# Kernel optimization log

Hardware: AMD Instinct MI355X
Metric: run time of the kernel (lower is better)

The kernel has to match this reference:

```python
import jax, jax.numpy as jnp
import numpy as np

CHAN = 128
IN_CHAN = 3
NB_OUT = 10
K = 2  # maxPoolKer


def affine_grid(theta, H, W):
    # theta: [C,2,3] -> grid [C,H,W,2], torch F.affine_grid align_corners=False
    xs = (2.0 * jnp.arange(W, dtype=jnp.float32) + 1.0) / W - 1.0
    ys = (2.0 * jnp.arange(H, dtype=jnp.float32) + 1.0) / H - 1.0
    gx, gy = jnp.meshgrid(xs, ys)  # [H,W]
    base = jnp.stack([gx, gy, jnp.ones_like(gx)], axis=-1)  # [H,W,3]
    return jnp.einsum('crk,hwk->chwr', theta, base)  # [...,0]=x, [...,1]=y


def grid_sample(img, grid):
    # img [M,H,W], grid [M,H,W,2]; bilinear, zeros padding, align_corners=False
    M, H, W = img.shape
    ix = ((grid[..., 0] + 1.0) * W - 1.0) * 0.5
    iy = ((grid[..., 1] + 1.0) * H - 1.0) * 0.5
    x0 = jnp.floor(ix)
    y0 = jnp.floor(iy)
    wx = ix - x0
    wy = iy - y0

    def tap(xi, yi):
        valid = (xi >= 0) & (xi <= W - 1) & (yi >= 0) & (yi <= H - 1)
        xc = jnp.clip(xi, 0, W - 1).astype(jnp.int32)
        yc = jnp.clip(yi, 0, H - 1).astype(jnp.int32)
        v = jax.vmap(lambda im, y, x: im[y, x])(img, yc, xc)
        return jnp.where(valid, v, 0.0)

    v00 = tap(x0, y0)
    v01 = tap(x0 + 1.0, y0)
    v10 = tap(x0, y0 + 1.0)
    v11 = tap(x0 + 1.0, y0 + 1.0)
    return (1.0 - wy) * ((1.0 - wx) * v00 + wx * v01) + wy * ((1.0 - wx) * v10 + wx * v11)


def geom_layer(x, geo, lin, box):
    # x [B,Ci,H,W]; lin [C,Ci]; geo,box [C,2,3]
    B, Ci, H, W = x.shape
    C = lin.shape[0]
    y = jnp.einsum('ci,bihw->bchw', lin, x)  # channel linear combine
    grid = affine_grid(geo, H, W)            # [C,H,W,2], shared across batch
    samp = jax.vmap(lambda yb: grid_sample(yb, grid))(y)  # [B,C,H,W]
    bgrid = affine_grid(box, H, W)
    boxm = grid_sample(jnp.ones((C, H, W), samp.dtype), bgrid)  # BoxPool mask
    return samp * boxm[None]


def maxpool_g(x, k):
    # MaxPool2d_G: depthwise box-filter conv -> argmax -> gather window from padded x
    B, C, H, W = x.shape
    ch, cw = H // k, W // k
    ker = jnp.ones((1, 1, ch, cw), x.dtype) / (ch + cw)
    xr = x.reshape(B * C, 1, H, W)
    conv = jax.lax.conv_general_dilated(
        xr, ker, (1, 1), [(ch // 2, ch // 2), (cw // 2, cw // 2)])
    conv = conv[:, :, :H, :W].reshape(B, C, H * W)
    argm = jnp.argmax(conv, axis=-1)
    r = argm // H  # original code uses origImgSize[0]; assumes square H==W
    c = argm % W
    padH, padW = H + H // k, W + W // k
    top = padH // 2 - H // 2
    left = padW // 2 - W // 2
    padded = jnp.zeros((B, C, padH, padW), x.dtype).at[:, :, top:top + H, left:left + W].set(x)
    r2 = r + H // (2 * k)
    c2 = c + W // (2 * k)
    ri = r2[..., None] + (jnp.arange(ch) - ch // 2)  # [B,C,ch]
    ci = c2[..., None] + (jnp.arange(cw) - cw // 2)  # [B,C,cw]
    gat = jax.vmap(jax.vmap(lambda p, rr, cc: p[rr[:, None], cc[None, :]]))(padded, ri, ci)
    return gat  # [B,C,ch,cw]


def setup_inputs() -> dict:
    key = jax.random.key(0)
    ks = jax.random.split(key, 12)
    eye = jnp.eye(3, dtype=jnp.float32)[:2]  # [2,3]
    x = jax.random.normal(ks[0], (8, IN_CHAN, 64, 64), dtype=jnp.float32)
    geo0 = eye[None] + 0.1 * jax.random.normal(ks[1], (CHAN, 2, 3), dtype=jnp.float32)
    lin0 = jax.random.uniform(ks[2], (CHAN, IN_CHAN), dtype=jnp.float32)
    box0 = eye[None] + 0.1 * jax.random.normal(ks[3], (CHAN, 2, 3), dtype=jnp.float32)
    geos = eye[None, None] + 0.1 * jax.random.normal(ks[4], (3, CHAN, 2, 3), dtype=jnp.float32)
    lins = jax.random.uniform(ks[5], (3, CHAN, CHAN), dtype=jnp.float32)
    boxes = eye[None, None] + 0.1 * jax.random.normal(ks[6], (3, CHAN, 2, 3), dtype=jnp.float32)
    bound = 1.0 / np.sqrt(CHAN)
    dense_w = jax.random.uniform(ks[7], (NB_OUT, CHAN), dtype=jnp.float32, minval=-bound, maxval=bound)
    dense_b = jax.random.uniform(ks[8], (NB_OUT,), dtype=jnp.float32, minval=-bound, maxval=bound)
    return {"x": x, "geo0": geo0, "lin0": lin0, "box0": box0,
            "geos": geos, "lins": lins, "boxes": boxes,
            "dense_w": dense_w, "dense_b": dense_b}


def reference(x, geo0, lin0, box0, geos, lins, boxes, dense_w, dense_b):
    h = geom_layer(x, geo0, lin0, box0)            # inLay: [8,128,64,64]
    h = geom_layer(h, geos[0], lins[0], boxes[0])  # layer 0
    h = maxpool_g(h, K)                            # layer 1 (maxPoolPos=1): [8,128,32,32]
    h = geom_layer(h, geos[1], lins[1], boxes[1])  # layer 2
    h = geom_layer(h, geos[2], lins[2], boxes[2])  # layer 3
    feat = h
    pooled = feat.mean(axis=-1).mean(axis=-1)      # [B,C]
    out = pooled @ dense_w.T + dense_b             # [B,nbOut]
    return out, feat
```

## Files before the change

kernel.cpp:

```cpp
#include <hip/hip_runtime.h>

#define BB 8
#define CC 128

__global__ __launch_bounds__(256) void inlay_sample_kernel(
    const float* __restrict__ x, const float* __restrict__ lin,
    const float* __restrict__ geo, const float* __restrict__ box,
    float* __restrict__ out) {
  const int H = 64, W = 64, HW = 4096;
  __shared__ __align__(16) float cp[64 * 68];
  int bc = blockIdx.x;
  int c = bc & (CC - 1);
  int b = bc >> 7;
  int tid = threadIdx.x;
  const float* xb = x + (size_t)b * 3 * HW;

  float w0 = lin[c * 3 + 0], w1 = lin[c * 3 + 1], w2 = lin[c * 3 + 2];

#pragma unroll
  for (int k = 0; k < 4; ++k) {
    int i4 = tid + k * 256;
    int base = i4 * 4;
    float4 f0 = *reinterpret_cast<const float4*>(&xb[base]);
    float4 f1 = *reinterpret_cast<const float4*>(&xb[HW + base]);
    float4 f2 = *reinterpret_cast<const float4*>(&xb[2 * HW + base]);
    float4 cv;
    cv.x = w0 * f0.x + w1 * f1.x + w2 * f2.x;
    cv.y = w0 * f0.y + w1 * f1.y + w2 * f2.y;
    cv.z = w0 * f0.z + w1 * f1.z + w2 * f2.z;
    cv.w = w0 * f0.w + w1 * f1.w + w2 * f2.w;
    int h = i4 >> 4, w = (i4 & 15) * 4;
    *reinterpret_cast<float4*>(&cp[h * 68 + w]) = cv;
  }
  __syncthreads();

  const float* g = geo + c * 6;
  const float* bx = box + c * 6;
  float g0 = g[0], g1 = g[1], g2 = g[2], g3 = g[3], g4 = g[4], g5 = g[5];
  float b0 = bx[0], b1 = bx[1], b2 = bx[2], b3 = bx[3], b4 = bx[4], b5 = bx[5];
  float* o = out + ((size_t)b * CC + c) * HW;

#pragma unroll
  for (int k = 0; k < 16; ++k) {
    int px = tid + k * 256;
    int h = px >> 6, w = px & 63;
    float xs = (2.0f * w + 1.0f) / W - 1.0f;
    float ys = (2.0f * h + 1.0f) / H - 1.0f;
    float gx = g0 * xs + g1 * ys + g2;
    float gy = g3 * xs + g4 * ys + g5;
    float ix = ((gx + 1.0f) * W - 1.0f) * 0.5f;
    float iy = ((gy + 1.0f) * H - 1.0f) * 0.5f;
    float x0 = floorf(ix), y0 = floorf(iy);
    float wx = ix - x0, wy = iy - y0;
    float v[2][2];
#pragma unroll
    for (int dy = 0; dy < 2; ++dy)
#pragma unroll
      for (int dx = 0; dx < 2; ++dx) {
        float xf = x0 + dx, yf = y0 + dy;
        bool valid = (xf >= 0.0f) && (xf <= 63.0f) && (yf >= 0.0f) && (yf <= 63.0f);
        int xi = (int)fminf(fmaxf(xf, 0.0f), 63.0f);
        int yi = (int)fminf(fmaxf(yf, 0.0f), 63.0f);
        v[dy][dx] = valid ? cp[yi * 68 + xi] : 0.0f;
      }
    float samp = (1.0f - wy) * ((1.0f - wx) * v[0][0] + wx * v[0][1]) +
                 wy * ((1.0f - wx) * v[1][0] + wx * v[1][1]);

    float bgx = b0 * xs + b1 * ys + b2;
    float bgy = b3 * xs + b4 * ys + b5;
    float bix = ((bgx + 1.0f) * W - 1.0f) * 0.5f;
    float biy = ((bgy + 1.0f) * H - 1.0f) * 0.5f;
    float bx0 = floorf(bix), by0 = floorf(biy);
    float bwx = bix - bx0, bwy = biy - by0;
    float m[2][2];
#pragma unroll
    for (int dy = 0; dy < 2; ++dy)
#pragma unroll
      for (int dx = 0; dx < 2; ++dx) {
        float xf = bx0 + dx, yf = by0 + dy;
        m[dy][dx] = ((xf >= 0.0f) && (xf <= 63.0f) && (yf >= 0.0f) && (yf <= 63.0f)) ? 1.0f : 0.0f;
      }
    float mask = (1.0f - bwy) * ((1.0f - bwx) * m[0][0] + bwx * m[0][1]) +
                 bwy * ((1.0f - bwx) * m[1][0] + bwx * m[1][1]);
    o[px] = samp * mask;
  }
}

__global__ __launch_bounds__(256) void gemm64_kernel(
    const float* __restrict__ lin, const float* __restrict__ x,
    float* __restrict__ y, int HW) {
  const int Ci = 128;
  __shared__ __align__(16) float As[16][68];
  __shared__ __align__(16) float Bs[16][64];
  int b = blockIdx.z;
  const float* xb = x + (size_t)b * Ci * HW;
  float* yb = y + (size_t)b * CC * HW;
  int tid = threadIdx.x;
  int tx = tid & 15, ty = tid >> 4;
  int row0 = blockIdx.y * 64;
  int col0 = blockIdx.x * 64;
  int m = tid >> 2, kq = (tid & 3) * 4;
  int kk = tid >> 4, n4 = (tid & 15) * 4;
  float acc[4][4] = {};
  float4 ra = *reinterpret_cast<const float4*>(&lin[(row0 + m) * Ci + kq]);
  float4 rb = *reinterpret_cast<const float4*>(&xb[(size_t)kk * HW + col0 + n4]);
  for (int k0 = 0; k0 < 128; k0 += 16) {
    __syncthreads();
    As[kq + 0][m] = ra.x; As[kq + 1][m] = ra.y; As[kq + 2][m] = ra.z; As[kq + 3][m] = ra.w;
    *reinterpret_cast<float4*>(&Bs[kk][n4]) = rb;
    __syncthreads();
    if (k0 + 16 < 128) {
      ra = *reinterpret_cast<const float4*>(&lin[(row0 + m) * Ci + k0 + 16 + kq]);
      rb = *reinterpret_cast<const float4*>(&xb[(size_t)(k0 + 16 + kk) * HW + col0 + n4]);
    }
#pragma unroll
    for (int kki = 0; kki < 16; ++kki) {
      float4 a4 = *reinterpret_cast<const float4*>(&As[kki][ty * 4]);
      float4 b4 = *reinterpret_cast<const float4*>(&Bs[kki][tx * 4]);
      float a[4] = {a4.x, a4.y, a4.z, a4.w};
      float bv[4] = {b4.x, b4.y, b4.z, b4.w};
#pragma unroll
      for (int i = 0; i < 4; i++)
#pragma unroll
        for (int j = 0; j < 4; j++) acc[i][j] += a[i] * bv[j];
    }
  }
#pragma unroll
  for (int i = 0; i < 4; i++) {
    float* yr = yb + (size_t)(row0 + ty * 4 + i) * HW + col0 + tx * 4;
    *reinterpret_cast<float4*>(yr) = make_float4(acc[i][0], acc[i][1], acc[i][2], acc[i][3]);
  }
}

__global__ __launch_bounds__(1024, 4) void sampmax_kernel(
    const float* __restrict__ y, const float* __restrict__ geo,
    const float* __restrict__ box, float* __restrict__ out) {
  __shared__ __align__(16) float sp[64 * 68];
  __shared__ __align__(16) float arena[64 * 100];
  __shared__ float wv[16];
  __shared__ int wi[16];
  __shared__ int am_s;
  float* pl = arena;
  float* cb = arena;

  int bc = blockIdx.x;
  int c = bc & (CC - 1);
  int b = bc >> 7;
  int tid = threadIdx.x;

  const float* plane = y + (size_t)bc * 4096;
  *reinterpret_cast<float4*>(&pl[tid * 4]) = *reinterpret_cast<const float4*>(&plane[tid * 4]);
  __syncthreads();

  {
    const float* g = geo + c * 6;
    const float* bx = box + c * 6;
    float g0 = g[0], g1 = g[1], g2 = g[2], g3 = g[3], g4 = g[4], g5 = g[5];
    float b0 = bx[0], b1 = bx[1], b2 = bx[2], b3 = bx[3], b4 = bx[4], b5 = bx[5];
#pragma unroll
    for (int k = 0; k < 4; ++k) {
      int px = tid + k * 1024;
      int h = px >> 6, w = px & 63;
      float xs = (2.0f * w + 1.0f) / 64.0f - 1.0f;
      float ys = (2.0f * h + 1.0f) / 64.0f - 1.0f;
      float gx = g0 * xs + g1 * ys + g2;
      float gy = g3 * xs + g4 * ys + g5;
      float ix = ((gx + 1.0f) * 64.0f - 1.0f) * 0.5f;
      float iy = ((gy + 1.0f) * 64.0f - 1.0f) * 0.5f;
      float x0 = floorf(ix), y0 = floorf(iy);
      float wx = ix - x0, wy = iy - y0;
      float v[2][2];
#pragma unroll
      for (int dy = 0; dy < 2; ++dy)
#pragma unroll
        for (int dx = 0; dx < 2; ++dx) {
          float xf = x0 + dx, yf = y0 + dy;
          bool valid = (xf >= 0.0f) && (xf <= 63.0f) && (yf >= 0.0f) && (yf <= 63.0f);
          int xi = (int)fminf(fmaxf(xf, 0.0f), 63.0f);
          int yi = (int)fminf(fmaxf(yf, 0.0f), 63.0f);
          v[dy][dx] = valid ? pl[yi * 64 + xi] : 0.0f;
        }
      float samp = (1.0f - wy) * ((1.0f - wx) * v[0][0] + wx * v[0][1]) +
                   wy * ((1.0f - wx) * v[1][0] + wx * v[1][1]);
      float bgx = b0 * xs + b1 * ys + b2;
      float bgy = b3 * xs + b4 * ys + b5;
      float bix = ((bgx + 1.0f) * 64.0f - 1.0f) * 0.5f;
      float biy = ((bgy + 1.0f) * 64.0f - 1.0f) * 0.5f;
      float bx0 = floorf(bix), by0 = floorf(biy);
      float bwx = bix - bx0, bwy = biy - by0;
      float m[2][2];
#pragma unroll
      for (int dy = 0; dy < 2; ++dy)
#pragma unroll
        for (int dx = 0; dx < 2; ++dx) {
          float xf = bx0 + dx, yf = by0 + dy;
          m[dy][dx] = ((xf >= 0.0f) && (xf <= 63.0f) && (yf >= 0.0f) && (yf <= 63.0f)) ? 1.0f : 0.0f;
        }
      float mask = (1.0f - bwy) * ((1.0f - bwx) * m[0][0] + bwx * m[0][1]) +
                   bwy * ((1.0f - bwx) * m[1][0] + bwx * m[1][1]);
      sp[h * 68 + w] = samp * mask;
    }
  }
  __syncthreads();

  if (tid < 256) {
    int strip = tid >> 4, w4 = (tid & 15) * 4;
    int h0 = strip * 4;
    float4 a0 = make_float4(0.f, 0.f, 0.f, 0.f), a1 = a0, a2 = a0, a3 = a0;
#pragma unroll
    for (int j = 0; j < 35; ++j) {
      int r = h0 + j - 16;
      bool valid = (r >= 0) && (r < 64);
      int rc = valid ? r : 0;
      float4 f = *reinterpret_cast<const float4*>(&sp[rc * 68 + w4]);
      f.x = valid ? f.x : 0.0f; f.y = valid ? f.y : 0.0f;
      f.z = valid ? f.z : 0.0f; f.w = valid ? f.w : 0.0f;
      if (j <= 31) { a0.x += f.x; a0.y += f.y; a0.z += f.z; a0.w += f.w; }
      if (j >= 1 && j <= 32) { a1.x += f.x; a1.y += f.y; a1.z += f.z; a1.w += f.w; }
      if (j >= 2 && j <= 33) { a2.x += f.x; a2.y += f.y; a2.z += f.z; a2.w += f.w; }
      if (j >= 3) { a3.x += f.x; a3.y += f.y; a3.z += f.z; a3.w += f.w; }
    }
    *reinterpret_cast<float4*>(&cb[(h0 + 0) * 100 + 16 + w4]) = a0;
    *reinterpret_cast<float4*>(&cb[(h0 + 1) * 100 + 16 + w4]) = a1;
    *reinterpret_cast<float4*>(&cb[(h0 + 2) * 100 + 16 + w4]) = a2;
    *reinterpret_cast<float4*>(&cb[(h0 + 3) * 100 + 16 + w4]) = a3;
  } else if (tid < 768) {
    int l = tid - 256;
    int row = l >> 3, gq = l & 7;
    int base = row * 100 + ((gq < 4) ? gq * 4 : 80 + (gq - 4) * 4);
    *reinterpret_cast<float4*>(&cb[base]) = make_float4(0.f, 0.f, 0.f, 0.f);
  }
  __syncthreads();

  float best = -3.402823466e+38f;
  int bidx = 0x7fffffff;
  {
    int h = tid >> 4, w4 = (tid & 15) * 4;
    float s0 = 0.f, s1 = 0.f, s2 = 0.f, s3 = 0.f;
#pragma unroll
    for (int q = 0; q < 9; ++q) {
      float4 f = *reinterpret_cast<const float4*>(&cb[h * 100 + w4 + 4 * q]);
      float fe[4] = {f.x, f.y, f.z, f.w};
#pragma unroll
      for (int e = 0; e < 4; ++e) {
        int u = 4 * q + e;
        if (u <= 31) s0 += fe[e];
        if (u >= 1 && u <= 32) s1 += fe[e];
        if (u >= 2 && u <= 33) s2 += fe[e];
        if (u >= 3 && u <= 34) s3 += fe[e];
      }
    }
    float sv[4] = {s0, s1, s2, s3};
#pragma unroll
    for (int d = 0; d < 4; ++d) {
      int i = (h << 6) + w4 + d;
      if (sv[d] > best) { best = sv[d]; bidx = i; }
    }
  }
#pragma unroll
  for (int off = 32; off > 0; off >>= 1) {
    float v2 = __shfl_down(best, off);
    int i2 = __shfl_down(bidx, off);
    if (v2 > best || (v2 == best && i2 < bidx)) { best = v2; bidx = i2; }
  }
  if ((tid & 63) == 0) { wv[tid >> 6] = best; wi[tid >> 6] = bidx; }
  __syncthreads();
  if (tid == 0) {
    float bv = wv[0]; int bi = wi[0];
#pragma unroll
    for (int k = 1; k < 16; ++k)
      if (wv[k] > bv || (wv[k] == bv && wi[k] < bi)) { bv = wv[k]; bi = wi[k]; }
    am_s = bi;
  }
  __syncthreads();

  int am = am_s;
  int r = am >> 6, cx = am & 63;
  float* o = out + (size_t)bc * 1024;
  {
    int oi = tid >> 5, oj = tid & 31;
    int rr = r + oi - 16, cj = cx + oj - 16;
    bool v = (rr >= 0) && (rr < 64) && (cj >= 0) && (cj < 64);
    int rrc = v ? rr : 0, cjc = v ? cj : 0;
    o[tid] = v ? sp[rrc * 68 + cjc] : 0.0f;
  }
}

template <bool POOL>
__global__ __launch_bounds__(256) void fused32_kernel(
    const float* __restrict__ lin, const float* __restrict__ x,
    const float* __restrict__ geo, const float* __restrict__ box,
    float* __restrict__ out, float* __restrict__ pooled) {
  const int H = 32, W = 32, HW = 1024;
  __shared__ __align__(16) float pls[2][1024];
  __shared__ float wred[8];
  int b = blockIdx.x & 7;
  int c0 = (blockIdx.x >> 3) * 2;
  int tid = threadIdx.x;
  const float* xb = x + (size_t)b * 128 * HW;
  const float* l0 = lin + (c0 + 0) * 128;
  const float* l1 = lin + (c0 + 1) * 128;
  int px4 = tid * 4;

  float4 acc0 = make_float4(0.f, 0.f, 0.f, 0.f);
  float4 acc1 = acc0;
#pragma unroll 8
  for (int k = 0; k < 128; ++k) {
    float4 xv = *reinterpret_cast<const float4*>(&xb[(size_t)k * HW + px4]);
    float s0 = l0[k], s1 = l1[k];
    acc0.x += s0 * xv.x; acc0.y += s0 * xv.y; acc0.z += s0 * xv.z; acc0.w += s0 * xv.w;
    acc1.x += s1 * xv.x; acc1.y += s1 * xv.y; acc1.z += s1 * xv.z; acc1.w += s1 * xv.w;
  }
  *reinterpret_cast<float4*>(&pls[0][px4]) = acc0;
  *reinterpret_cast<float4*>(&pls[1][px4]) = acc1;
  __syncthreads();

  float psum[2] = {0.f, 0.f};
#pragma unroll
  for (int c = 0; c < 2; ++c) {
    const float* g = geo + (c0 + c) * 6;
    const float* bxp = box + (c0 + c) * 6;
    float g0 = g[0], g1 = g[1], g2 = g[2], g3 = g[3], g4 = g[4], g5 = g[5];
    float b0 = bxp[0], b1 = bxp[1], b2 = bxp[2], b3 = bxp[3], b4 = bxp[4], b5 = bxp[5];
    float* o = out + ((size_t)b * CC + c0 + c) * HW;
    const float* pl = pls[c];
#pragma unroll
    for (int k = 0; k < 4; ++k) {
      int px = tid + k * 256;
      int h = px >> 5, w = px & 31;
      float xs = (2.0f * w + 1.0f) / W - 1.0f;
      float ys = (2.0f * h + 1.0f) / H - 1.0f;
      float gx = g0 * xs + g1 * ys + g2;
      float gy = g3 * xs + g4 * ys + g5;
      float ix = ((gx + 1.0f) * W - 1.0f) * 0.5f;
      float iy = ((gy + 1.0f) * H - 1.0f) * 0.5f;
      float x0 = floorf(ix), y0 = floorf(iy);
      float wx = ix - x0, wy = iy - y0;
      float v[2][2];
#pragma unroll
      for (int dy = 0; dy < 2; ++dy)
#pragma unroll
        for (int dx = 0; dx < 2; ++dx) {
          float xf = x0 + dx, yf = y0 + dy;
          bool valid = (xf >= 0.0f) && (xf <= 31.0f) && (yf >= 0.0f) && (yf <= 31.0f);
          int xi = (int)fminf(fmaxf(xf, 0.0f), 31.0f);
          int yi = (int)fminf(fmaxf(yf, 0.0f), 31.0f);
          v[dy][dx] = valid ? pl[yi * 32 + xi] : 0.0f;
        }
      float samp = (1.0f - wy) * ((1.0f - wx) * v[0][0] + wx * v[0][1]) +
                   wy * ((1.0f - wx) * v[1][0] + wx * v[1][1]);
      float bgx = b0 * xs + b1 * ys + b2;
      float bgy = b3 * xs + b4 * ys + b5;
      float bix = ((bgx + 1.0f) * W - 1.0f) * 0.5f;
      float biy = ((bgy + 1.0f) * H - 1.0f) * 0.5f;
      float bx0 = floorf(bix), by0 = floorf(biy);
      float bwx = bix - bx0, bwy = biy - by0;
      float m[2][2];
#pragma unroll
      for (int dy = 0; dy < 2; ++dy)
#pragma unroll
        for (int dx = 0; dx < 2; ++dx) {
          float xf = bx0 + dx, yf = by0 + dy;
          m[dy][dx] = ((xf >= 0.0f) && (xf <= 31.0f) && (yf >= 0.0f) && (yf <= 31.0f)) ? 1.0f : 0.0f;
        }
      float mask = (1.0f - bwy) * ((1.0f - bwx) * m[0][0] + bwx * m[0][1]) +
                   bwy * ((1.0f - bwx) * m[1][0] + bwx * m[1][1]);
      float res = samp * mask;
      o[px] = res;
      if (POOL) psum[c] += res;
    }
  }
  if (POOL) {
    int lane = tid & 63, wid = tid >> 6;
#pragma unroll
    for (int c = 0; c < 2; ++c) {
      float r = psum[c];
#pragma unroll
      for (int off = 32; off > 0; off >>= 1) r += __shfl_down(r, off);
      if (lane == 0) wred[c * 4 + wid] = r;
    }
    __syncthreads();
    if (tid < 2) {
      float t = wred[tid * 4] + wred[tid * 4 + 1] + wred[tid * 4 + 2] + wred[tid * 4 + 3];
      pooled[b * CC + c0 + tid] = t * (1.0f / 1024.0f);
    }
  }
}

__global__ __launch_bounds__(128) void dense_kernel(
    const float* __restrict__ pooled, const float* __restrict__ w,
    const float* __restrict__ bias, float* __restrict__ out) {
  int t = threadIdx.x;
  if (t < 80) {
    int b = t / 10, o = t % 10;
    float s = bias[o];
    const float* pb = pooled + b * 128;
    const float* wo = w + o * 128;
    for (int c = 0; c < 128; ++c) s += pb[c] * wo[c];
    out[b * 10 + o] = s;
  }
}

extern "C" void kernel_launch(void* const* d_in, const int* in_sizes, int n_in,
                              void* d_out, int out_size, void* d_ws, size_t ws_size,
                              hipStream_t stream) {
  const float* x     = (const float*)d_in[0];
  const float* geo0  = (const float*)d_in[1];
  const float* lin0  = (const float*)d_in[2];
  const float* box0  = (const float*)d_in[3];
  const float* geos  = (const float*)d_in[4];
  const float* lins  = (const float*)d_in[5];
  const float* boxes = (const float*)d_in[6];
  const float* dw    = (const float*)d_in[7];
  const float* db    = (const float*)d_in[8];

  float* out  = (float*)d_out;
  float* feat = out + 80;
  float* ws   = (float*)d_ws;
  float* ws0  = ws;
  float* ws1  = ws + 4194304;
  float* pooled = ws + 8388608;

  inlay_sample_kernel<<<dim3(BB * CC), 256, 0, stream>>>(x, lin0, geo0, box0, ws1);
  gemm64_kernel<<<dim3(64, 2, BB), 256, 0, stream>>>(lins, ws1, ws0, 4096);
  sampmax_kernel<<<dim3(BB * CC), 1024, 0, stream>>>(ws0, geos, boxes, ws1);
  fused32_kernel<false><<<dim3(512), 256, 0, stream>>>(lins + 16384, ws1, geos + 768, boxes + 768, ws0, nullptr);
  fused32_kernel<true><<<dim3(512), 256, 0, stream>>>(lins + 32768, ws0, geos + 1536, boxes + 1536, feat, pooled);
  dense_kernel<<<1, 128, 0, stream>>>(pooled, dw, db, out);
}
```

Before: 163.2 us.

## Fuse dense head via atomics, sliding-window box filter, remap block indices, 4-channel fused32

Removes the separate dense kernel. The inlay kernel now seeds the output with the bias, and the last fused32 kernel adds per-channel pooled contributions through atomicAdd. The box-filter in sampmax now uses sliding-window subtraction instead of four masked accumulators. Block indices are remapped so that batch varies fastest across inlay, gemm and sampmax, and fused32 now handles four channels per 512-thread block using float2 loads. The atomics make the summation order nondeterministic, and the head output depends on the inlay kernel running first to write the bias.

Measured after the change: 167.9 us. 2.9% more time.

```diff
diff --git a/kernel.cpp b/kernel.cpp
--- a/kernel.cpp
+++ b/kernel.cpp
@@ -6,13 +6,15 @@
 __global__ __launch_bounds__(256) void inlay_sample_kernel(
     const float* __restrict__ x, const float* __restrict__ lin,
     const float* __restrict__ geo, const float* __restrict__ box,
-    float* __restrict__ out) {
+    const float* __restrict__ db, float* __restrict__ out,
+    float* __restrict__ head) {
   const int H = 64, W = 64, HW = 4096;
   __shared__ __align__(16) float cp[64 * 68];
   int bc = blockIdx.x;
-  int c = bc & (CC - 1);
-  int b = bc >> 7;
+  int b = bc & 7;
+  int c = bc >> 3;
   int tid = threadIdx.x;
+  if (bc == 0 && tid < 80) head[tid] = db[tid % 10];
   const float* xb = x + (size_t)b * 3 * HW;
 
   float w0 = lin[c * 3 + 0], w1 = lin[c * 3 + 1], w2 = lin[c * 3 + 2];
@@ -92,13 +94,15 @@
   const int Ci = 128;
   __shared__ __align__(16) float As[16][68];
   __shared__ __align__(16) float Bs[16][64];
-  int b = blockIdx.z;
+  int bx = blockIdx.x;
+  int b = bx & 7;
+  int t = bx >> 3;
+  int row0 = (t & 1) * 64;
+  int col0 = (t >> 1) * 64;
   const float* xb = x + (size_t)b * Ci * HW;
   float* yb = y + (size_t)b * CC * HW;
   int tid = threadIdx.x;
   int tx = tid & 15, ty = tid >> 4;
-  int row0 = blockIdx.y * 64;
-  int col0 = blockIdx.x * 64;
   int m = tid >> 2, kq = (tid & 3) * 4;
   int kk = tid >> 4, n4 = (tid & 15) * 4;
   float acc[4][4] = {};
@@ -144,11 +148,11 @@
   float* cb = arena;
 
   int bc = blockIdx.x;
-  int c = bc & (CC - 1);
-  int b = bc >> 7;
+  int b = bc & 7;
+  int c = bc >> 3;
   int tid = threadIdx.x;
 
-  const float* plane = y + (size_t)bc * 4096;
+  const float* plane = y + ((size_t)b * CC + c) * 4096;
   *reinterpret_cast<float4*>(&pl[tid * 4]) = *reinterpret_cast<const float4*>(&plane[tid * 4]);
   __syncthreads();
 
@@ -206,24 +210,34 @@
   if (tid < 256) {
     int strip = tid >> 4, w4 = (tid & 15) * 4;
     int h0 = strip * 4;
-    float4 a0 = make_float4(0.f, 0.f, 0.f, 0.f), a1 = a0, a2 = a0, a3 = a0;
-#pragma unroll
-    for (int j = 0; j < 35; ++j) {
+    float4 a = make_float4(0.f, 0.f, 0.f, 0.f);
+    float4 keep0 = a, keep1 = a, keep2 = a;
+#pragma unroll
+    for (int j = 0; j < 32; ++j) {
       int r = h0 + j - 16;
       bool valid = (r >= 0) && (r < 64);
       int rc = valid ? r : 0;
       float4 f = *reinterpret_cast<const float4*>(&sp[rc * 68 + w4]);
       f.x = valid ? f.x : 0.0f; f.y = valid ? f.y : 0.0f;
       f.z = valid ? f.z : 0.0f; f.w = valid ? f.w : 0.0f;
-      if (j <= 31) { a0.x += f.x; a0.y += f.y; a0.z += f.z; a0.w += f.w; }
-      if (j >= 1 && j <= 32) { a1.x += f.x; a1.y += f.y; a1.z += f.z; a1.w += f.w; }
-      if (j >= 2 && j <= 33) { a2.x += f.x; a2.y += f.y; a2.z += f.z; a2.w += f.w; }
-      if (j >= 3) { a3.x += f.x; a3.y += f.y; a3.z += f.z; a3.w += f.w; }
-    }
-    *reinterpret_cast<float4*>(&cb[(h0 + 0) * 100 + 16 + w4]) = a0;
-    *reinterpret_cast<float4*>(&cb[(h0 + 1) * 100 + 16 + w4]) = a1;
-    *reinterpret_cast<float4*>(&cb[(h0 + 2) * 100 + 16 + w4]) = a2;
-    *reinterpret_cast<float4*>(&cb[(h0 + 3) * 100 + 16 + w4]) = a3;
+      if (j == 0) keep0 = f;
+      if (j == 1) keep1 = f;
+      if (j == 2) keep2 = f;
+      a.x += f.x; a.y += f.y; a.z += f.z; a.w += f.w;
+    }
+    *reinterpret_cast<float4*>(&cb[(h0 + 0) * 100 + 16 + w4]) = a;
+#pragma unroll
+    for (int j = 32; j < 35; ++j) {
+      int r = h0 + j - 16;
+      bool valid = (r < 64);
+      int rc = valid ? r : 0;
+      float4 f = *reinterpret_cast<const float4*>(&sp[rc * 68 + w4]);
+      f.x = valid ? f.x : 0.0f; f.y = valid ? f.y : 0.0f;
+      f.z = valid ? f.z : 0.0f; f.w = valid ? f.w : 0.0f;
+      float4 kp = (j == 32) ? keep0 : ((j == 33) ? keep1 : keep2);
+      a.x += f.x - kp.x; a.y += f.y - kp.y; a.z += f.z - kp.z; a.w += f.w - kp.w;
+      *reinterpret_cast<float4*>(&cb[(h0 + j - 31) * 100 + 16 + w4]) = a;
+    }
   } else if (tid < 768) {
     int l = tid - 256;
     int row = l >> 3, gq = l & 7;
@@ -236,20 +250,17 @@
   int bidx = 0x7fffffff;
   {
     int h = tid >> 4, w4 = (tid & 15) * 4;
-    float s0 = 0.f, s1 = 0.f, s2 = 0.f, s3 = 0.f;
-#pragma unroll
-    for (int q = 0; q < 9; ++q) {
+    float s0 = 0.f, k0 = 0.f, k1 = 0.f, k2 = 0.f;
+#pragma unroll
+    for (int q = 0; q < 8; ++q) {
       float4 f = *reinterpret_cast<const float4*>(&cb[h * 100 + w4 + 4 * q]);
-      float fe[4] = {f.x, f.y, f.z, f.w};
-#pragma unroll
-      for (int e = 0; e < 4; ++e) {
-        int u = 4 * q + e;
-        if (u <= 31) s0 += fe[e];
-        if (u >= 1 && u <= 32) s1 += fe[e];
-        if (u >= 2 && u <= 33) s2 += fe[e];
-        if (u >= 3 && u <= 34) s3 += fe[e];
-      }
-    }
+      if (q == 0) { k0 = f.x; k1 = f.y; k2 = f.z; }
+      s0 += f.x; s0 += f.y; s0 += f.z; s0 += f.w;
+    }
+    float4 ft = *reinterpret_cast<const float4*>(&cb[h * 100 + w4 + 32]);
+    float s1 = s0 - k0 + ft.x;
+    float s2 = s1 - k1 + ft.y;
+    float s3 = s2 - k2 + ft.z;
     float sv[4] = {s0, s1, s2, s3};
 #pragma unroll
     for (int d = 0; d < 4; ++d) {
@@ -276,7 +287,7 @@
 
   int am = am_s;
   int r = am >> 6, cx = am & 63;
-  float* o = out + (size_t)bc * 1024;
+  float* o = out + ((size_t)b * CC + c) * 1024;
   {
     int oi = tid >> 5, oj = tid & 31;
     int rr = r + oi - 16, cj = cx + oj - 16;
@@ -287,37 +298,44 @@
 }
 
 template <bool POOL>
-__global__ __launch_bounds__(256) void fused32_kernel(
+__global__ __launch_bounds__(512) void fused32_kernel(
     const float* __restrict__ lin, const float* __restrict__ x,
     const float* __restrict__ geo, const float* __restrict__ box,
-    float* __restrict__ out, float* __restrict__ pooled) {
+    float* __restrict__ out, const float* __restrict__ dw,
+    float* __restrict__ head) {
   const int H = 32, W = 32, HW = 1024;
-  __shared__ __align__(16) float pls[2][1024];
-  __shared__ float wred[8];
+  __shared__ __align__(16) float pls[4][1024];
+  __shared__ float wred[32];
+  __shared__ float wsum[4];
   int b = blockIdx.x & 7;
-  int c0 = (blockIdx.x >> 3) * 2;
+  int c0 = (blockIdx.x >> 3) * 4;
   int tid = threadIdx.x;
   const float* xb = x + (size_t)b * 128 * HW;
   const float* l0 = lin + (c0 + 0) * 128;
   const float* l1 = lin + (c0 + 1) * 128;
-  int px4 = tid * 4;
-
-  float4 acc0 = make_float4(0.f, 0.f, 0.f, 0.f);
-  float4 acc1 = acc0;
+  const float* l2 = lin + (c0 + 2) * 128;
+  const float* l3 = lin + (c0 + 3) * 128;
+  int px2 = tid * 2;
+
+  float2 a0 = make_float2(0.f, 0.f), a1 = a0, a2 = a0, a3 = a0;
 #pragma unroll 8
   for (int k = 0; k < 128; ++k) {
-    float4 xv = *reinterpret_cast<const float4*>(&xb[(size_t)k * HW + px4]);
-    float s0 = l0[k], s1 = l1[k];
-    acc0.x += s0 * xv.x; acc0.y += s0 * xv.y; acc0.z += s0 * xv.z; acc0.w += s0 * xv.w;
-    acc1.x += s1 * xv.x; acc1.y += s1 * xv.y; acc1.z += s1 * xv.z; acc1.w += s1 * xv.w;
-  }
-  *reinterpret_cast<float4*>(&pls[0][px4]) = acc0;
-  *reinterpret_cast<float4*>(&pls[1][px4]) = acc1;
-  __syncthreads();
-
-  float psum[2] = {0.f, 0.f};
-#pragma unroll
-  for (int c = 0; c < 2; ++c) {
+    float2 xv = *reinterpret_cast<const float2*>(&xb[(size_t)k * HW + px2]);
+    float s0 = l0[k], s1 = l1[k], s2 = l2[k], s3 = l3[k];
+    a0.x += s0 * xv.x; a0.y += s0 * xv.y;
+    a1.x += s1 * xv.x; a1.y += s1 * xv.y;
+    a2.x += s2 * xv.x; a2.y += s2 * xv.y;
+    a3.x += s3 * xv.x; a3.y += s3 * xv.y;
+  }
+  *reinterpret_cast<float2*>(&pls[0][px2]) = a0;
+  *reinterpret_cast<float2*>(&pls[1][px2]) = a1;
+  *reinterpret_cast<float2*>(&pls[2][px2]) = a2;
+  *reinterpret_cast<float2*>(&pls[3][px2]) = a3;
+  __syncthreads();
+
+  float psum[4] = {0.f, 0.f, 0.f, 0.f};
+#pragma unroll
+  for (int c = 0; c < 4; ++c) {
     const float* g = geo + (c0 + c) * 6;
     const float* bxp = box + (c0 + c) * 6;
     float g0 = g[0], g1 = g[1], g2 = g[2], g3 = g[3], g4 = g[4], g5 = g[5];
@@ -325,8 +343,8 @@
     float* o = out + ((size_t)b * CC + c0 + c) * HW;
     const float* pl = pls[c];
 #pragma unroll
-    for (int k = 0; k < 4; ++k) {
-      int px = tid + k * 256;
+    for (int k = 0; k < 2; ++k) {
+      int px = tid + k * 512;
       int h = px >> 5, w = px & 31;
       float xs = (2.0f * w + 1.0f) / W - 1.0f;
       float ys = (2.0f * h + 1.0f) / H - 1.0f;
@@ -373,31 +391,26 @@
   if (POOL) {
     int lane = tid & 63, wid = tid >> 6;
 #pragma unroll
-    for (int c = 0; c < 2; ++c) {
+    for (int c = 0; c < 4; ++c) {
       float r = psum[c];
 #pragma unroll
       for (int off = 32; off > 0; off >>= 1) r += __shfl_down(r, off);
-      if (lane == 0) wred[c * 4 + wid] = r;
+      if (lane == 0) wred[c * 8 + wid] = r;
     }
     __syncthreads();
-    if (tid < 2) {
-      float t = wred[tid * 4] + wred[tid * 4 + 1] + wred[tid * 4 + 2] + wred[tid * 4 + 3];
-      pooled[b * CC + c0 + tid] = t * (1.0f / 1024.0f);
-    }
-  }
-}
-
-__global__ __launch_bounds__(128) void dense_kernel(
-    const float* __restrict__ pooled, const float* __restrict__ w,
-    const float* __restrict__ bias, float* __restrict__ out) {
-  int t = threadIdx.x;
-  if (t < 80) {
-    int b = t / 10, o = t % 10;
-    float s = bias[o];
-    const float* pb = pooled + b * 128;
-    const float* wo = w + o * 128;
-    for (int c = 0; c < 128; ++c) s += pb[c] * wo[c];
-    out[b * 10 + o] = s;
+    if (tid < 4) {
+      float t = 0.f;
+#pragma unroll
+      for (int w = 0; w < 8; ++w) t += wred[tid * 8 + w];
+      wsum[tid] = t * (1.0f / 1024.0f);
+    }
+    __syncthreads();
+    if (tid < 10) {
+      float s = 0.f;
+#pragma unroll
+      for (int c = 0; c < 4; ++c) s += wsum[c] * dw[tid * 128 + c0 + c];
+      atomicAdd(&head[b * 10 + tid], s);
+    }
   }
 }
 
@@ -419,12 +432,10 @@
   float* ws   = (float*)d_ws;
   float* ws0  = ws;
   float* ws1  = ws + 4194304;
-  float* pooled = ws + 8388608;
-
-  inlay_sample_kernel<<<dim3(BB * CC), 256, 0, stream>>>(x, lin0, geo0, box0, ws1);
-  gemm64_kernel<<<dim3(64, 2, BB), 256, 0, stream>>>(lins, ws1, ws0, 4096);
+
+  inlay_sample_kernel<<<dim3(BB * CC), 256, 0, stream>>>(x, lin0, geo0, box0, db, ws1, out);
+  gemm64_kernel<<<dim3(1024), 256, 0, stream>>>(lins, ws1, ws0, 4096);
   sampmax_kernel<<<dim3(BB * CC), 1024, 0, stream>>>(ws0, geos, boxes, ws1);
-  fused32_kernel<false><<<dim3(512), 256, 0, stream>>>(lins + 16384, ws1, geos + 768, boxes + 768, ws0, nullptr);
-  fused32_kernel<true><<<dim3(512), 256, 0, stream>>>(lins + 32768, ws0, geos + 1536, boxes + 1536, feat, pooled);
-  dense_kernel<<<1, 128, 0, stream>>>(pooled, dw, db, out);
+  fused32_kernel<false><<<dim3(256), 512, 0, stream>>>(lins + 16384, ws1, geos + 768, boxes + 768, ws0, nullptr, nullptr);
+  fused32_kernel<true><<<dim3(256), 512, 0, stream>>>(lins + 32768, ws0, geos + 1536, boxes + 1536, feat, dw, out);
 }
```
